# Kernel optimization log

Hardware: AMD Instinct MI355X
Metric: run time of the kernel (lower is better)

Reference implementation:

```python
import jax, jax.numpy as jnp
import numpy as np

N_NODES = 100000
N_EDGES = 800000
N_GRAPHS = 64
N_ETYPES = 4
D = 150
HID = 512
PASSES = 5


def setup_inputs() -> dict:
    key = jax.random.key(0)
    ks = jax.random.split(key, 16)
    s = 0.1
    return {
        "nodes": jax.random.normal(ks[0], (N_NODES, D), jnp.float32),
        "problem_class": jax.random.normal(ks[1], (N_GRAPHS, 1), jnp.float32),
        "edge_src": jax.random.randint(ks[2], (N_EDGES,), 0, N_NODES, jnp.int32),
        "edge_dst": jax.random.randint(ks[3], (N_EDGES,), 0, N_NODES, jnp.int32),
        "edge_type": jax.random.randint(ks[4], (N_EDGES,), 0, N_ETYPES, jnp.int32),
        "graph_ids": jnp.sort(jax.random.randint(ks[5], (N_NODES,), 0, N_GRAPHS, jnp.int32)),
        "W_e": jax.random.normal(ks[6], (N_ETYPES, D, D), jnp.float32) * s,
        "b_e": jax.random.normal(ks[7], (N_ETYPES, D), jnp.float32) * s,
        "w_ih": jax.random.normal(ks[8], (3 * D, D), jnp.float32) * s,
        "w_hh": jax.random.normal(ks[9], (3 * D, D), jnp.float32) * s,
        "b_ih": jax.random.normal(ks[10], (3 * D,), jnp.float32) * s,
        "b_hh": jax.random.normal(ks[11], (3 * D,), jnp.float32) * s,
        "fc1_w": jax.random.normal(ks[12], (D + 1, HID), jnp.float32) * s,
        "fc1_b": jax.random.normal(ks[13], (HID,), jnp.float32) * s,
        "fc2_w": jax.random.normal(ks[14], (HID, 10), jnp.float32) * s,
        "fc2_b": jax.random.normal(ks[15], (10,), jnp.float32) * s,
    }


def _gru_cell(x, h, w_ih, w_hh, b_ih, b_hh):
    # torch.nn.GRUCell math, gate order (r, z, n)
    gi = x @ w_ih.T + b_ih
    gh = h @ w_hh.T + b_hh
    i_r, i_z, i_n = jnp.split(gi, 3, axis=1)
    h_r, h_z, h_n = jnp.split(gh, 3, axis=1)
    r = jax.nn.sigmoid(i_r + h_r)
    z = jax.nn.sigmoid(i_z + h_z)
    n = jnp.tanh(i_n + r * h_n)
    return (1.0 - z) * n + z * h


def reference(nodes, problem_class, edge_src, edge_dst, edge_type, graph_ids,
              W_e, b_e, w_ih, w_hh, b_ih, b_hh, fc1_w, fc1_b, fc2_w, fc2_b):
    n_nodes = nodes.shape[0]
    n_graphs = problem_class.shape[0]
    n_types = W_e.shape[0]

    # in-degree per edge type (for the per-edge Linear bias contribution)
    type_onehot = jax.nn.one_hot(edge_type, n_types, dtype=nodes.dtype)  # [E, T]
    deg = jax.ops.segment_sum(type_onehot, edge_dst, num_segments=n_nodes)  # [N, T]
    bias_inc = deg @ b_e  # [N, D] = sum_t deg_t * b_t

    h = nodes
    for _ in range(PASSES):
        h_src = h[edge_src]  # [E, D] gather
        inc = bias_inc
        for t in range(n_types):
            # aggregate first, apply the edge-type Linear after (linearity)
            agg = jax.ops.segment_sum(
                jnp.where((edge_type == t)[:, None], h_src, 0.0),
                edge_dst, num_segments=n_nodes)  # [N, D]
            inc = inc + agg @ W_e[t].T
        h = _gru_cell(inc, h, w_ih, w_hh, b_ih, b_hh)

    # graph readout: sum nodes, log, nan -> 0, relu
    g = jax.ops.segment_sum(h, graph_ids, num_segments=n_graphs)  # [B, D]
    l = jnp.log(g)
    l = jax.nn.relu(jnp.where(jnp.isnan(l), 0.0, l))
    x = jnp.concatenate([l, problem_class], axis=1)  # [B, D+1]
    x = jax.nn.leaky_relu(x @ fc1_w + fc1_b)
    return x @ fc2_w + fc2_b
```

## Files before the change

kernel.cpp:

```cpp
#include <hip/hip_runtime.h>
#include <hip/hip_bf16.h>
#include <cstdint>
#include <cstddef>

#define NN 100000
#define NE 800000
#define NG 64
#define NT 4
#define DD 150
#define HS 160
#define HIDN 512
#define NPASS 5
#define NBINS (NN*NT)
#define RPB 16

typedef short  s8v  __attribute__((ext_vector_type(8)));
typedef float  f32x4 __attribute__((ext_vector_type(4)));

static __device__ __forceinline__ float sigmoidf_(float x){ return 1.f/(1.f+expf(-x)); }
static __device__ __forceinline__ short f2bf(float x){
  __hip_bfloat16 b = __float2bfloat16(x);
  return *(short*)&b;
}
static __device__ __forceinline__ float bf2f(short s){
  union { unsigned u; float f; } v; v.u = ((unsigned)(unsigned short)s) << 16; return v.f;
}
static __device__ __forceinline__ void split_bf(float x, short& hi, short& lo){
  hi = f2bf(x);
  lo = f2bf(x - bf2f(hi));
}


__global__ void count_kernel(const int* __restrict__ dst, const int* __restrict__ typ,
                             unsigned* __restrict__ deg){
  int e = blockIdx.x*256 + threadIdx.x;
  if (e < NE) atomicAdd(&deg[dst[e]*NT + typ[e]], 1u);
}

__device__ unsigned block_excl_base(unsigned threadSum){
  const int tid = threadIdx.x;
  const int lane = tid & 63, wid = tid >> 6;
  unsigned s = threadSum;
  #pragma unroll
  for (int d = 1; d < 64; d <<= 1){ unsigned t = __shfl_up(s, d); if (lane >= d) s += t; }
  __shared__ unsigned wsum[4];
  if (lane == 63) wsum[wid] = s;
  __syncthreads();
  unsigned base = 0;
  for (int w = 0; w < wid; w++) base += wsum[w];
  return base + s - threadSum;
}

__global__ void scan_reduce(const unsigned* __restrict__ deg, unsigned* __restrict__ bsum){
  const int base = blockIdx.x*1024 + threadIdx.x*4;
  unsigned s = 0;
  #pragma unroll
  for (int i = 0; i < 4; i++){ const int idx = base+i; if (idx < NBINS) s += deg[idx]; }
  #pragma unroll
  for (int d = 1; d < 64; d <<= 1) s += __shfl_down(s, d);
  __shared__ unsigned ws4[4];
  const int lane = threadIdx.x & 63, wid = threadIdx.x >> 6;
  if (lane == 0) ws4[wid] = s;
  __syncthreads();
  if (threadIdx.x == 0) bsum[blockIdx.x] = ws4[0]+ws4[1]+ws4[2]+ws4[3];
}

__global__ void scan_block(unsigned* bsum, int n){
  const int tid = threadIdx.x;
  unsigned v[4]; unsigned s = 0;
  #pragma unroll
  for (int i = 0; i < 4; i++){ const int idx = tid*4+i; v[i] = (idx < n) ? bsum[idx] : 0u; s += v[i]; }
  unsigned run = block_excl_base(s);
  #pragma unroll
  for (int i = 0; i < 4; i++){ const int idx = tid*4+i; if (idx < n) bsum[idx] = run; run += v[i]; }
}

__global__ void scan_final(const unsigned* __restrict__ deg, const unsigned* __restrict__ bsum,
                           unsigned* __restrict__ off){
  const int tid = threadIdx.x;
  const int base0 = blockIdx.x*1024 + tid*4;
  unsigned v[4]; unsigned s = 0;
  #pragma unroll
  for (int i = 0; i < 4; i++){ const int idx = base0+i; v[i] = (idx < NBINS) ? deg[idx] : 0u; s += v[i]; }
  unsigned run = block_excl_base(s) + bsum[blockIdx.x];
  #pragma unroll
  for (int i = 0; i < 4; i++){ const int idx = base0+i; if (idx < NBINS) off[idx] = run; run += v[i]; }
  if (blockIdx.x == 0 && tid == 0) off[NBINS] = NE;
}

__global__ void scatter_sort(const int* __restrict__ src, const int* __restrict__ dst,
                             const int* __restrict__ typ, unsigned* __restrict__ cur,
                             int* __restrict__ srcSorted){
  int e = blockIdx.x*256 + threadIdx.x;
  if (e < NE){
    const int bin = dst[e]*NT + typ[e];
    const unsigned p = atomicAdd(&cur[bin], 1u);
    srcSorted[p] = src[e];
  }
}

__global__ void init_h(const float* __restrict__ nodes, float* __restrict__ h0){
  const long long idx = (long long)blockIdx.x*256 + threadIdx.x;
  if (idx >= (long long)NN*HS) return;
  const int row = (int)(idx / HS), col = (int)(idx % HS);
  float v = 0.f;
  if (col < DD) v = nodes[(size_t)row*DD + col];
  h0[idx] = v;
}

__global__ void build_bfrag_msg(const float* __restrict__ W, unsigned short* __restrict__ out){
  const int idx = blockIdx.x*256 + threadIdx.x;
  if (idx >= NT*5*10*2*512) return;
  const int w = idx & 511;
  int r = idx >> 9;
  const int c = r % 2;  r /= 2;
  const int i = r % 10; r /= 10;
  const int s = r % 5;  const int t = r / 5;
  const int l = w >> 3, j = w & 7;
  const int n  = 16*i + (l & 15);
  const int kk = 32*s + (l >> 4)*8 + j;
  float v = 0.f;
  if (n < DD && kk < DD) v = W[(size_t)(t*DD + n)*DD + kk];
  short hi, lo; split_bf(v, hi, lo);
  out[(size_t)((t*5 + s)*20 + i*2 + c)*512 + w] = (unsigned short)(c ? lo : hi);
}

__global__ void build_bfrag_gru(const float* __restrict__ w_ih, const float* __restrict__ w_hh,
                                unsigned short* __restrict__ out){
  const int idx = blockIdx.x*256 + threadIdx.x;
  if (idx >= 10*2*3*2*5*512) return;
  const int w = idx & 511;
  int r = idx >> 9;
  const int s = r % 5;    r /= 5;
  const int c = r % 2;    r /= 2;
  const int pp = r % 3;   r /= 3;
  const int half = r % 2; const int iT = r / 2;
  const int P = half*3 + pp;
  const int g = P >> 1;
  const float* W = (P & 1) ? w_hh : w_ih;
  const int l = w >> 3, j = w & 7;
  const int n  = 16*iT + (l & 15);
  const int kk = 32*s + (l >> 4)*8 + j;
  float v = 0.f;
  if (n < DD && kk < DD) v = W[(size_t)(g*DD + n)*DD + kk];
  short hi, lo; split_bf(v, hi, lo);
  out[(size_t)((iT*2 + half)*30 + pp*10 + c*5 + s)*512 + w] = (unsigned short)(c ? lo : hi);
}

#define MFMA3(acc, ahi, alo, bhi, blo) \
  acc = __builtin_amdgcn_mfma_f32_16x16x32_bf16(ahi, bhi, acc, 0,0,0); \
  acc = __builtin_amdgcn_mfma_f32_16x16x32_bf16(alo, bhi, acc, 0,0,0); \
  acc = __builtin_amdgcn_mfma_f32_16x16x32_bf16(ahi, blo, acc, 0,0,0);

__global__ __launch_bounds__(512, 2) void msg_kernel(
    const float* __restrict__ h, const int* __restrict__ srcS,
    const unsigned* __restrict__ off, const unsigned* __restrict__ deg,
    const float* __restrict__ b_e,
    const unsigned short* __restrict__ BfE2,
    float* __restrict__ inc)
{
  __shared__ short Bs[2][20*512];
  const int tid = threadIdx.x, wave = tid >> 6, l = tid & 63;
  const int m = l & 15, q = l >> 4, q8 = q*8;
  const int arow = blockIdx.x*128 + wave*16 + m;
  const bool av = (arow < NN);
  const int lb8 = l*8;

  f32x4 acc[10];
  #pragma unroll
  for (int i = 0; i < 10; i++) acc[i] = (f32x4)(0.0f);

  #pragma unroll
  for (int k2 = 0; k2 < 3; k2++){
    const int c = tid + k2*512;
    if (c < 1280) *(s8v*)(&Bs[0][c*8]) = *(const s8v*)(BfE2 + (size_t)c*8);
  }
  __syncthreads();

  s8v sv[3];
  for (int t = 0; t < NT; t++){
    #pragma unroll
    for (int k2 = 0; k2 < 3; k2++){
      const int c = tid + k2*512;
      if (c < 1280) sv[k2] = *(const s8v*)(BfE2 + (size_t)(t*5 + 1)*10240 + (size_t)c*8);
    }

    float a[5][8];
    #pragma unroll
    for (int s = 0; s < 5; s++)
      #pragma unroll
      for (int j = 0; j < 8; j++) a[s][j] = 0.f;

    int lo = 0, hi = 0;
    if (av){ const int bin = arow*NT + t; lo = (int)off[bin]; hi = (int)off[bin+1]; }
    int e = lo;
    int i0 = (e   < hi) ? srcS[e]   : 0;
    int i1 = (e+1 < hi) ? srcS[e+1] : -1;
    while (e < hi){
      const int n0 = (e+2 < hi) ? srcS[e+2] : 0;
      const int n1 = (e+3 < hi) ? srcS[e+3] : -1;
      const float* p0 = h + (size_t)i0*HS + q8;
      const float* p1 = h + (size_t)(i1 < 0 ? 0 : i1)*HS + q8;
      const float w1 = (i1 < 0) ? 0.f : 1.f;
      f32x4 v[10], u[10];
      #pragma unroll
      for (int s = 0; s < 5; s++){
        v[2*s]   = *(const f32x4*)(p0 + 32*s);
        v[2*s+1] = *(const f32x4*)(p0 + 32*s + 4);
      }
      #pragma unroll
      for (int s = 0; s < 5; s++){
        u[2*s]   = *(const f32x4*)(p1 + 32*s);
        u[2*s+1] = *(const f32x4*)(p1 + 32*s + 4);
      }
      #pragma unroll
      for (int s = 0; s < 5; s++){
        #pragma unroll
        for (int j = 0; j < 4; j++){
          a[s][j]   += v[2*s][j];
          a[s][j]   = fmaf(w1, u[2*s][j], a[s][j]);
          a[s][4+j] += v[2*s+1][j];
          a[s][4+j] = fmaf(w1, u[2*s+1][j], a[s][4+j]);
        }
      }
      e += 2; i0 = n0; i1 = n1;
    }

    s8v af_hi[5], af_lo[5];
    #pragma unroll
    for (int s = 0; s < 5; s++)
      #pragma unroll
      for (int j = 0; j < 8; j++){
        short h2, l2; split_bf(a[s][j], h2, l2);
        af_hi[s][j] = h2; af_lo[s][j] = l2;
      }

    #pragma unroll
    for (int st = 0; st < 5; st++){
      const int sidx = t*5 + st;
      const short* bsr = &Bs[sidx & 1][0];
      #pragma unroll
      for (int i = 0; i < 10; i++){
        const s8v bh = *(const s8v*)(bsr + (i*2+0)*512 + lb8);
        const s8v bl = *(const s8v*)(bsr + (i*2+1)*512 + lb8);
        MFMA3(acc[i], af_hi[st], af_lo[st], bh, bl)
      }
      if (sidx + 1 < 20){
        short* bsw = &Bs[(sidx+1) & 1][0];
        #pragma unroll
        for (int k2 = 0; k2 < 3; k2++){
          const int c = tid + k2*512;
          if (c < 1280) *(s8v*)(bsw + c*8) = sv[k2];
        }
      }
      if (st < 4 && sidx + 2 < 20){
        #pragma unroll
        for (int k2 = 0; k2 < 3; k2++){
          const int c = tid + k2*512;
          if (c < 1280) sv[k2] = *(const s8v*)(BfE2 + (size_t)(sidx+2)*10240 + (size_t)c*8);
        }
      }
      __syncthreads();
    }
  }

  const int crow0 = blockIdx.x*128 + wave*16 + q*4;
  #pragma unroll
  for (int r = 0; r < 4; r++){
    const int crow = crow0 + r;
    if (crow < NN){
      const uint4 dg = *(const uint4*)(&deg[crow*NT]);
      const float d0=(float)dg.x, d1=(float)dg.y, d2=(float)dg.z, d3=(float)dg.w;
      float* op = inc + (size_t)crow*HS;
      #pragma unroll
      for (int i = 0; i < 10; i++){
        const int c = 16*i + m;
        float val = 0.f;
        if (c < DD)
          val = acc[i][r] + fmaf(d0, b_e[c], fmaf(d1, b_e[DD+c],
                  fmaf(d2, b_e[2*DD+c], d3*b_e[3*DD+c])));
        op[c] = val;
      }
    }
  }
}

__global__ __launch_bounds__(512, 2) void gru_kernel(
    const float* __restrict__ h, float* __restrict__ incnext,
    const unsigned short* __restrict__ BfG,
    const float* __restrict__ b_ih, const float* __restrict__ b_hh)
{
  __shared__ short Bs[2][30*512];
  const int tid = threadIdx.x, wave = tid >> 6, l = tid & 63;
  const int m = l & 15, q = l >> 4, q8 = q*8;
  const int arow = blockIdx.x*128 + wave*16 + m;
  const bool av = (arow < NN);
  const int lb8 = l*8;
  const int crow0 = blockIdx.x*128 + wave*16 + q*4;

  s8v afi_h[5], afi_l[5], afh_h[5], afh_l[5];
  {
    const float* ip = incnext + (size_t)(av ? arow : 0)*HS;
    const float* hp = h       + (size_t)(av ? arow : 0)*HS;
    #pragma unroll
    for (int s = 0; s < 5; s++){
      const int b = 32*s + q8;
      const f32x4 x0 = *(const f32x4*)(ip + b), x1 = *(const f32x4*)(ip + b + 4);
      const f32x4 y0 = *(const f32x4*)(hp + b), y1 = *(const f32x4*)(hp + b + 4);
      #pragma unroll
      for (int j = 0; j < 4; j++){
        short h2, l2;
        split_bf(x0[j], h2, l2); afi_h[s][j]   = h2; afi_l[s][j]   = l2;
        split_bf(x1[j], h2, l2); afi_h[s][4+j] = h2; afi_l[s][4+j] = l2;
        split_bf(y0[j], h2, l2); afh_h[s][j]   = h2; afh_l[s][j]   = l2;
        split_bf(y1[j], h2, l2); afh_h[s][4+j] = h2; afh_l[s][4+j] = l2;
      }
    }
  }

  #pragma unroll
  for (int k2 = 0; k2 < 4; k2++){
    const int c = tid + k2*512;
    if (c < 1920) *(s8v*)(&Bs[0][c*8]) = *(const s8v*)(BfG + (size_t)c*8);
  }
  __syncthreads();

  s8v sv[4];
  #pragma unroll
  for (int k2 = 0; k2 < 4; k2++){
    const int c = tid + k2*512;
    if (c < 1920) sv[k2] = *(const s8v*)(BfG + (size_t)15360 + (size_t)c*8);
  }

  f32x4 aR=(f32x4)(0.f), aZ=(f32x4)(0.f), aIN=(f32x4)(0.f), aHN=(f32x4)(0.f);
  float hv[4] = {0.f,0.f,0.f,0.f};

  for (int k = 0; k < 20; k++){
    const int iT = k >> 1, half = k & 1;
    const int d = 16*iT + m;
    if (half == 0){
      aR = (f32x4)(0.f); aZ = (f32x4)(0.f); aIN = (f32x4)(0.f); aHN = (f32x4)(0.f);
      #pragma unroll
      for (int r = 0; r < 4; r++){
        hv[r] = 0.f;
        if (crow0 + r < NN && d < DD) hv[r] = h[(size_t)(crow0+r)*HS + d];
      }
    }

    const short* bsr = &Bs[k & 1][0];
    if (half == 0){
      #pragma unroll
      for (int s = 0; s < 5; s++){
        const s8v b0h = *(const s8v*)(bsr + (0*10 + s)*512 + lb8);
        const s8v b0l = *(const s8v*)(bsr + (0*10 + 5 + s)*512 + lb8);
        MFMA3(aR, afi_h[s], afi_l[s], b0h, b0l)
        const s8v b1h = *(const s8v*)(bsr + (1*10 + s)*512 + lb8);
        const s8v b1l = *(const s8v*)(bsr + (1*10 + 5 + s)*512 + lb8);
        MFMA3(aR, afh_h[s], afh_l[s], b1h, b1l)
        const s8v b2h = *(const s8v*)(bsr + (2*10 + s)*512 + lb8);
        const s8v b2l = *(const s8v*)(bsr + (2*10 + 5 + s)*512 + lb8);
        MFMA3(aZ, afi_h[s], afi_l[s], b2h, b2l)
      }
    } else {
      #pragma unroll
      for (int s = 0; s < 5; s++){
        const s8v b0h = *(const s8v*)(bsr + (0*10 + s)*512 + lb8);
        const s8v b0l = *(const s8v*)(bsr + (0*10 + 5 + s)*512 + lb8);
        MFMA3(aZ, afh_h[s], afh_l[s], b0h, b0l)
        const s8v b1h = *(const s8v*)(bsr + (1*10 + s)*512 + lb8);
        const s8v b1l = *(const s8v*)(bsr + (1*10 + 5 + s)*512 + lb8);
        MFMA3(aIN, afi_h[s], afi_l[s], b1h, b1l)
        const s8v b2h = *(const s8v*)(bsr + (2*10 + s)*512 + lb8);
        const s8v b2l = *(const s8v*)(bsr + (2*10 + 5 + s)*512 + lb8);
        MFMA3(aHN, afh_h[s], afh_l[s], b2h, b2l)
      }
    }

    if (k < 19){
      short* bsw = &Bs[(k+1) & 1][0];
      #pragma unroll
      for (int k2 = 0; k2 < 4; k2++){
        const int c = tid + k2*512;
        if (c < 1920) *(s8v*)(bsw + c*8) = sv[k2];
      }
    }
    if (k < 18){
      #pragma unroll
      for (int k2 = 0; k2 < 4; k2++){
        const int c = tid + k2*512;
        if (c < 1920) sv[k2] = *(const s8v*)(BfG + (size_t)(k+2)*15360 + (size_t)c*8);
      }
    }

    if (half == 1 && d < DD){
      const float br   = b_ih[d]    + b_hh[d];
      const float bz   = b_ih[DD+d] + b_hh[DD+d];
      const float bin2 = b_ih[2*DD+d];
      const float bhn  = b_hh[2*DD+d];
      #pragma unroll
      for (int r = 0; r < 4; r++){
        const int crow = crow0 + r;
        if (crow < NN){
          const float rr = sigmoidf_(aR[r] + br);
          const float zz = sigmoidf_(aZ[r] + bz);
          const float nn = tanhf(aIN[r] + bin2 + rr*(aHN[r] + bhn));
          incnext[(size_t)crow*HS + d] = (1.f - zz)*nn + zz*hv[r];
        }
      }
    }
    __syncthreads();
  }
}

__global__ void readout1(const float* __restrict__ h, const int* __restrict__ gids,
                         float* __restrict__ part){
  const int g = blockIdx.x >> 4, s = blockIdx.x & (RPB-1);
  const int tid = threadIdx.x;
  __shared__ int sb[2];
  if (tid < 2){
    const int target = g + tid;
    int lo = 0, hi = NN;
    while (lo < hi){ const int mid = (lo+hi) >> 1; if (gids[mid] < target) lo = mid+1; else hi = mid; }
    sb[tid] = lo;
  }
  __syncthreads();
  const int lo = sb[0], hi = sb[1];
  const int len = hi - lo;
  const int per = (len + RPB - 1) / RPB;
  const int nlo = lo + s*per;
  const int nhi = (nlo + per < hi) ? (nlo + per) : hi;
  if (tid < DD){
    float acc = 0.f;
    for (int n = nlo; n < nhi; n++) acc += h[(size_t)n*HS + tid];
    part[(size_t)blockIdx.x*DD + tid] = acc;
  }
}

__global__ void readout2(const float* __restrict__ part, const float* __restrict__ pclass,
                         float* __restrict__ xbuf){
  const int g = blockIdx.x, tid = threadIdx.x;
  if (tid < DD){
    float acc = 0.f;
    #pragma unroll
    for (int s = 0; s < RPB; s++) acc += part[(size_t)(g*RPB + s)*DD + tid];
    float l = logf(acc);
    if (isnan(l)) l = 0.f;
    l = fmaxf(l, 0.f);
    xbuf[g*(DD+1)+tid] = l;
  }
  if (tid == DD) xbuf[g*(DD+1)+DD] = pclass[g];
}

__global__ void fc1_kernel(const float* __restrict__ xbuf, const float* __restrict__ w,
                           const float* __restrict__ b, float* __restrict__ hid){
  const int g = blockIdx.x, tid = threadIdx.x;
  __shared__ float xs[DD+1];
  if (tid < DD+1) xs[tid] = xbuf[g*(DD+1)+tid];
  __syncthreads();
  float acc = b[tid];
  for (int k = 0; k < DD+1; k++) acc = fmaf(xs[k], w[k*HIDN + tid], acc);
  hid[g*HIDN + tid] = (acc > 0.f) ? acc : 0.01f*acc;
}

__global__ void fc2_kernel(const float* __restrict__ hid, const float* __restrict__ w,
                           const float* __restrict__ b, float* __restrict__ out){
  const int g = blockIdx.x, tid = threadIdx.x;
  __shared__ float hs[HIDN];
  for (int i = tid; i < HIDN; i += 64) hs[i] = hid[g*HIDN + i];
  __syncthreads();
  if (tid < 10){
    float acc = b[tid];
    for (int k = 0; k < HIDN; k++) acc = fmaf(hs[k], w[k*10 + tid], acc);
    out[g*10 + tid] = acc;
  }
}

extern "C" void kernel_launch(void* const* d_in, const int* in_sizes, int n_in,
                              void* d_out, int out_size, void* d_ws, size_t ws_size,
                              hipStream_t stream)
{
  (void)in_sizes; (void)n_in; (void)out_size; (void)ws_size;
  const float* nodes  = (const float*)d_in[0];
  const float* pclass = (const float*)d_in[1];
  const int*   esrc   = (const int*)d_in[2];
  const int*   edst   = (const int*)d_in[3];
  const int*   etyp   = (const int*)d_in[4];
  const int*   gids   = (const int*)d_in[5];
  const float* W_e    = (const float*)d_in[6];
  const float* b_e    = (const float*)d_in[7];
  const float* w_ih   = (const float*)d_in[8];
  const float* w_hh   = (const float*)d_in[9];
  const float* b_ih   = (const float*)d_in[10];
  const float* b_hh   = (const float*)d_in[11];
  const float* fc1w   = (const float*)d_in[12];
  const float* fc1b   = (const float*)d_in[13];
  const float* fc2w   = (const float*)d_in[14];
  const float* fc2b   = (const float*)d_in[15];
  float* out = (float*)d_out;

  char* p = (char*)d_ws;
  auto alloc = [&](size_t bytes)->char* {
    char* r = p; p += ((bytes + 255) & ~(size_t)255); return r;
  };
  float*    h0   = (float*)alloc((size_t)NN*HS*4);
  float*    h1   = (float*)alloc((size_t)NN*HS*4);
  unsigned* deg  = (unsigned*)alloc((size_t)NBINS*4);
  unsigned* off  = (unsigned*)alloc((size_t)(NBINS+1)*4);
  unsigned* cur  = (unsigned*)alloc((size_t)NBINS*4);
  unsigned* bsum = (unsigned*)alloc(4096);
  int*      srcS = (int*)alloc((size_t)NE*4);
  unsigned short* BfE2 = (unsigned short*)alloc((size_t)20*20*512*2);
  unsigned short* BfG  = (unsigned short*)alloc((size_t)20*30*512*2);
  float*    part = (float*)alloc((size_t)NG*RPB*DD*4);
  float*    xbuf = (float*)alloc((size_t)NG*(DD+1)*4);
  float*    hidb = (float*)alloc((size_t)NG*HIDN*4);

  hipMemsetAsync(deg, 0, (size_t)NBINS*4, stream);
  count_kernel<<<(NE+255)/256, 256, 0, stream>>>(edst, etyp, deg);
  const int SCB = (NBINS + 1023)/1024;
  scan_reduce<<<SCB, 256, 0, stream>>>(deg, bsum);
  scan_block<<<1, 256, 0, stream>>>(bsum, SCB);
  scan_final<<<SCB, 256, 0, stream>>>(deg, bsum, off);
  hipMemcpyAsync(cur, off, (size_t)NBINS*4, hipMemcpyDeviceToDevice, stream);
  scatter_sort<<<(NE+255)/256, 256, 0, stream>>>(esrc, edst, etyp, cur, srcS);
  build_bfrag_msg<<<(NT*5*10*2*512+255)/256, 256, 0, stream>>>(W_e, BfE2);
  build_bfrag_gru<<<(10*2*3*2*5*512+255)/256, 256, 0, stream>>>(w_ih, w_hh, BfG);
  init_h<<<(int)(((long long)NN*HS + 255)/256), 256, 0, stream>>>(nodes, h0);

  float* hb[2] = {h0, h1};
  const int grows = (NN + 127)/128;
  for (int pass = 0; pass < NPASS; pass++){
    const float* hc = hb[pass & 1];
    float*       hn = hb[(pass + 1) & 1];
    msg_kernel<<<grows, 512, 0, stream>>>(hc, srcS, off, deg, b_e, BfE2, hn);
    gru_kernel<<<grows, 512, 0, stream>>>(hc, hn, BfG, b_ih, b_hh);
  }

  readout1<<<NG*RPB, 256, 0, stream>>>(hb[NPASS & 1], gids, part);
  readout2<<<NG, 256, 0, stream>>>(part, pclass, xbuf);
  fc1_kernel<<<NG, HIDN, 0, stream>>>(xbuf, fc1w, fc1b, hidb);
  fc2_kernel<<<NG, 64, 0, stream>>>(hidb, fc2w, fc2b, out);
}
```

Baseline: 2.252 ms.

## Shrink msg_kernel blocks to 256 threads and re-split GRU weight staging into thirds

The message kernel now runs 256-thread blocks covering 64 rows, with launch bounds allowing four blocks per CU. Each thread stages five weight chunks instead of three, with the bounds checks removed. The GRU kernel's B-fragment layout is regrouped into three 20-fragment parts per 16-column tile (r, z, n gates), so the LDS double buffer shrinks from 30 to 20 fragments at the cost of 30 pipeline steps and barriers instead of 20. The aim is more resident blocks and lower LDS use, but it adds more weight restaging per row and more synchronisation.

```diff
diff --git a/kernel.cpp b/kernel.cpp
--- a/kernel.cpp
+++ b/kernel.cpp
@@ -128,14 +128,14 @@
 __global__ void build_bfrag_gru(const float* __restrict__ w_ih, const float* __restrict__ w_hh,
                                 unsigned short* __restrict__ out){
   const int idx = blockIdx.x*256 + threadIdx.x;
-  if (idx >= 10*2*3*2*5*512) return;
+  if (idx >= 10*3*2*2*5*512) return;
   const int w = idx & 511;
   int r = idx >> 9;
   const int s = r % 5;    r /= 5;
   const int c = r % 2;    r /= 2;
-  const int pp = r % 3;   r /= 3;
-  const int half = r % 2; const int iT = r / 2;
-  const int P = half*3 + pp;
+  const int u = r % 2;    r /= 2;
+  const int part = r % 3; const int iT = r / 3;
+  const int P = part*2 + u;
   const int g = P >> 1;
   const float* W = (P & 1) ? w_hh : w_ih;
   const int l = w >> 3, j = w & 7;
@@ -144,7 +144,7 @@
   float v = 0.f;
   if (n < DD && kk < DD) v = W[(size_t)(g*DD + n)*DD + kk];
   short hi, lo; split_bf(v, hi, lo);
-  out[(size_t)((iT*2 + half)*30 + pp*10 + c*5 + s)*512 + w] = (unsigned short)(c ? lo : hi);
+  out[(size_t)((iT*3 + part)*20 + u*10 + c*5 + s)*512 + w] = (unsigned short)(c ? lo : hi);
 }
 
 #define MFMA3(acc, ahi, alo, bhi, blo) \
@@ -152,7 +152,7 @@
   acc = __builtin_amdgcn_mfma_f32_16x16x32_bf16(alo, bhi, acc, 0,0,0); \
   acc = __builtin_amdgcn_mfma_f32_16x16x32_bf16(ahi, blo, acc, 0,0,0);
 
-__global__ __launch_bounds__(512, 2) void msg_kernel(
+__global__ __launch_bounds__(256, 4) void msg_kernel(
     const float* __restrict__ h, const int* __restrict__ srcS,
     const unsigned* __restrict__ off, const unsigned* __restrict__ deg,
     const float* __restrict__ b_e,
@@ -162,7 +162,7 @@
   __shared__ short Bs[2][20*512];
   const int tid = threadIdx.x, wave = tid >> 6, l = tid & 63;
   const int m = l & 15, q = l >> 4, q8 = q*8;
-  const int arow = blockIdx.x*128 + wave*16 + m;
+  const int arow = blockIdx.x*64 + wave*16 + m;
   const bool av = (arow < NN);
   const int lb8 = l*8;
 
@@ -171,18 +171,18 @@
   for (int i = 0; i < 10; i++) acc[i] = (f32x4)(0.0f);
 
   #pragma unroll
-  for (int k2 = 0; k2 < 3; k2++){
-    const int c = tid + k2*512;
-    if (c < 1280) *(s8v*)(&Bs[0][c*8]) = *(const s8v*)(BfE2 + (size_t)c*8);
-  }
-  __syncthreads();
-
-  s8v sv[3];
+  for (int k2 = 0; k2 < 5; k2++){
+    const int c = tid + k2*256;
+    *(s8v*)(&Bs[0][c*8]) = *(const s8v*)(BfE2 + (size_t)c*8);
+  }
+  __syncthreads();
+
+  s8v sv[5];
   for (int t = 0; t < NT; t++){
     #pragma unroll
-    for (int k2 = 0; k2 < 3; k2++){
-      const int c = tid + k2*512;
-      if (c < 1280) sv[k2] = *(const s8v*)(BfE2 + (size_t)(t*5 + 1)*10240 + (size_t)c*8);
+    for (int k2 = 0; k2 < 5; k2++){
+      const int c = tid + k2*256;
+      sv[k2] = *(const s8v*)(BfE2 + (size_t)(t*5 + 1)*10240 + (size_t)c*8);
     }
 
     float a[5][8];
@@ -248,23 +248,23 @@
       if (sidx + 1 < 20){
         short* bsw = &Bs[(sidx+1) & 1][0];
         #pragma unroll
-        for (int k2 = 0; k2 < 3; k2++){
-          const int c = tid + k2*512;
-          if (c < 1280) *(s8v*)(bsw + c*8) = sv[k2];
+        for (int k2 = 0; k2 < 5; k2++){
+          const int c = tid + k2*256;
+          *(s8v*)(bsw + c*8) = sv[k2];
         }
       }
       if (st < 4 && sidx + 2 < 20){
         #pragma unroll
-        for (int k2 = 0; k2 < 3; k2++){
-          const int c = tid + k2*512;
-          if (c < 1280) sv[k2] = *(const s8v*)(BfE2 + (size_t)(sidx+2)*10240 + (size_t)c*8);
+        for (int k2 = 0; k2 < 5; k2++){
+          const int c = tid + k2*256;
+          sv[k2] = *(const s8v*)(BfE2 + (size_t)(sidx+2)*10240 + (size_t)c*8);
         }
       }
       __syncthreads();
     }
   }
 
-  const int crow0 = blockIdx.x*128 + wave*16 + q*4;
+  const int crow0 = blockIdx.x*64 + wave*16 + q*4;
   #pragma unroll
   for (int r = 0; r < 4; r++){
     const int crow = crow0 + r;
@@ -290,7 +290,7 @@
     const unsigned short* __restrict__ BfG,
     const float* __restrict__ b_ih, const float* __restrict__ b_hh)
 {
-  __shared__ short Bs[2][30*512];
+  __shared__ short Bs[2][20*512];
   const int tid = threadIdx.x, wave = tid >> 6, l = tid & 63;
   const int m = l & 15, q = l >> 4, q8 = q*8;
   const int arow = blockIdx.x*128 + wave*16 + m;
@@ -319,26 +319,26 @@
   }
 
   #pragma unroll
-  for (int k2 = 0; k2 < 4; k2++){
+  for (int k2 = 0; k2 < 3; k2++){
     const int c = tid + k2*512;
-    if (c < 1920) *(s8v*)(&Bs[0][c*8]) = *(const s8v*)(BfG + (size_t)c*8);
-  }
-  __syncthreads();
-
-  s8v sv[4];
-  #pragma unroll
-  for (int k2 = 0; k2 < 4; k2++){
+    if (c < 1280) *(s8v*)(&Bs[0][c*8]) = *(const s8v*)(BfG + (size_t)c*8);
+  }
+  __syncthreads();
+
+  s8v sv[3];
+  #pragma unroll
+  for (int k2 = 0; k2 < 3; k2++){
     const int c = tid + k2*512;
-    if (c < 1920) sv[k2] = *(const s8v*)(BfG + (size_t)15360 + (size_t)c*8);
+    if (c < 1280) sv[k2] = *(const s8v*)(BfG + (size_t)10240 + (size_t)c*8);
   }
 
   f32x4 aR=(f32x4)(0.f), aZ=(f32x4)(0.f), aIN=(f32x4)(0.f), aHN=(f32x4)(0.f);
   float hv[4] = {0.f,0.f,0.f,0.f};
 
-  for (int k = 0; k < 20; k++){
-    const int iT = k >> 1, half = k & 1;
+  for (int k = 0; k < 30; k++){
+    const int iT = k/3, part = k - 3*iT;
     const int d = 16*iT + m;
-    if (half == 0){
+    if (part == 0){
       aR = (f32x4)(0.f); aZ = (f32x4)(0.f); aIN = (f32x4)(0.f); aHN = (f32x4)(0.f);
       #pragma unroll
       for (int r = 0; r < 4; r++){
@@ -348,51 +348,41 @@
     }
 
     const short* bsr = &Bs[k & 1][0];
-    if (half == 0){
-      #pragma unroll
-      for (int s = 0; s < 5; s++){
-        const s8v b0h = *(const s8v*)(bsr + (0*10 + s)*512 + lb8);
-        const s8v b0l = *(const s8v*)(bsr + (0*10 + 5 + s)*512 + lb8);
+    #pragma unroll
+    for (int s = 0; s < 5; s++){
+      const s8v b0h = *(const s8v*)(bsr + (     s)*512 + lb8);
+      const s8v b0l = *(const s8v*)(bsr + ( 5 + s)*512 + lb8);
+      const s8v b1h = *(const s8v*)(bsr + (10 + s)*512 + lb8);
+      const s8v b1l = *(const s8v*)(bsr + (15 + s)*512 + lb8);
+      if (part == 0){
         MFMA3(aR, afi_h[s], afi_l[s], b0h, b0l)
-        const s8v b1h = *(const s8v*)(bsr + (1*10 + s)*512 + lb8);
-        const s8v b1l = *(const s8v*)(bsr + (1*10 + 5 + s)*512 + lb8);
         MFMA3(aR, afh_h[s], afh_l[s], b1h, b1l)
-        const s8v b2h = *(const s8v*)(bsr + (2*10 + s)*512 + lb8);
-        const s8v b2l = *(const s8v*)(bsr + (2*10 + 5 + s)*512 + lb8);
-        MFMA3(aZ, afi_h[s], afi_l[s], b2h, b2l)
-      }
-    } else {
-      #pragma unroll
-      for (int s = 0; s < 5; s++){
-        const s8v b0h = *(const s8v*)(bsr + (0*10 + s)*512 + lb8);
-        const s8v b0l = *(const s8v*)(bsr + (0*10 + 5 + s)*512 + lb8);
-        MFMA3(aZ, afh_h[s], afh_l[s], b0h, b0l)
-        const s8v b1h = *(const s8v*)(bsr + (1*10 + s)*512 + lb8);
-        const s8v b1l = *(const s8v*)(bsr + (1*10 + 5 + s)*512 + lb8);
-        MFMA3(aIN, afi_h[s], afi_l[s], b1h, b1l)
-        const s8v b2h = *(const s8v*)(bsr + (2*10 + s)*512 + lb8);
-        const s8v b2l = *(const s8v*)(bsr + (2*10 + 5 + s)*512 + lb8);
-        MFMA3(aHN, afh_h[s], afh_l[s], b2h, b2l)
-      }
-    }
-
-    if (k < 19){
+      } else if (part == 1){
+        MFMA3(aZ, afi_h[s], afi_l[s], b0h, b0l)
+        MFMA3(aZ, afh_h[s], afh_l[s], b1h, b1l)
+      } else {
+        MFMA3(aIN, afi_h[s], afi_l[s], b0h, b0l)
+        MFMA3(aHN, afh_h[s], afh_l[s], b1h, b1l)
+      }
+    }
+
+    if (k < 29){
       short* bsw = &Bs[(k+1) & 1][0];
       #pragma unroll
-      for (int k2 = 0; k2 < 4; k2++){
+      for (int k2 = 0; k2 < 3; k2++){
         const int c = tid + k2*512;
-        if (c < 1920) *(s8v*)(bsw + c*8) = sv[k2];
-      }
-    }
-    if (k < 18){
-      #pragma unroll
-      for (int k2 = 0; k2 < 4; k2++){
+        if (c < 1280) *(s8v*)(bsw + c*8) = sv[k2];
+      }
+    }
+    if (k < 28){
+      #pragma unroll
+      for (int k2 = 0; k2 < 3; k2++){
         const int c = tid + k2*512;
-        if (c < 1920) sv[k2] = *(const s8v*)(BfG + (size_t)(k+2)*15360 + (size_t)c*8);
-      }
-    }
-
-    if (half == 1 && d < DD){
+        if (c < 1280) sv[k2] = *(const s8v*)(BfG + (size_t)(k+2)*10240 + (size_t)c*8);
+      }
+    }
+
+    if (part == 2 && d < DD){
       const float br   = b_ih[d]    + b_hh[d];
       const float bz   = b_ih[DD+d] + b_hh[DD+d];
       const float bin2 = b_ih[2*DD+d];
@@ -510,7 +500,7 @@
   unsigned* bsum = (unsigned*)alloc(4096);
   int*      srcS = (int*)alloc((size_t)NE*4);
   unsigned short* BfE2 = (unsigned short*)alloc((size_t)20*20*512*2);
-  unsigned short* BfG  = (unsigned short*)alloc((size_t)20*30*512*2);
+  unsigned short* BfG  = (unsigned short*)alloc((size_t)30*20*512*2);
   float*    part = (float*)alloc((size_t)NG*RPB*DD*4);
   float*    xbuf = (float*)alloc((size_t)NG*(DD+1)*4);
   float*    hidb = (float*)alloc((size_t)NG*HIDN*4);
@@ -524,16 +514,17 @@
   hipMemcpyAsync(cur, off, (size_t)NBINS*4, hipMemcpyDeviceToDevice, stream);
   scatter_sort<<<(NE+255)/256, 256, 0, stream>>>(esrc, edst, etyp, cur, srcS);
   build_bfrag_msg<<<(NT*5*10*2*512+255)/256, 256, 0, stream>>>(W_e, BfE2);
-  build_bfrag_gru<<<(10*2*3*2*5*512+255)/256, 256, 0, stream>>>(w_ih, w_hh, BfG);
+  build_bfrag_gru<<<(10*3*2*2*5*512+255)/256, 256, 0, stream>>>(w_ih, w_hh, BfG);
   init_h<<<(int)(((long long)NN*HS + 255)/256), 256, 0, stream>>>(nodes, h0);
 
   float* hb[2] = {h0, h1};
-  const int grows = (NN + 127)/128;
+  const int growsM = (NN + 63)/64;
+  const int growsG = (NN + 127)/128;
   for (int pass = 0; pass < NPASS; pass++){
     const float* hc = hb[pass & 1];
     float*       hn = hb[(pass + 1) & 1];
-    msg_kernel<<<grows, 512, 0, stream>>>(hc, srcS, off, deg, b_e, BfE2, hn);
-    gru_kernel<<<grows, 512, 0, stream>>>(hc, hn, BfG, b_ih, b_hh);
+    msg_kernel<<<growsM, 256, 0, stream>>>(hc, srcS, off, deg, b_e, BfE2, hn);
+    gru_kernel<<<growsG, 512, 0, stream>>>(hc, hn, BfG, b_ih, b_hh);
   }
 
   readout1<<<NG*RPB, 256, 0, stream>>>(hb[NPASS & 1], gids, part);
```

Result: slower. 2.736 ms (+21.5%).
